# Performance work log

Measured on AMD Instinct MI355X. Metric: run time of the kernel, lower is better.

## Reference

```python
import jax, jax.numpy as jnp
import numpy as np

B, S, D, H = 64, 512, 1024, 1024


def setup_inputs() -> dict:
    key = jax.random.key(0)
    k1, k2, k3 = jax.random.split(key, 3)
    scale = 1.0 / np.sqrt(H)
    U = jax.random.normal(k1, (B, S, D), dtype=jnp.float32)
    W_ih = jax.random.normal(k2, (3 * H, D), dtype=jnp.float32) * scale
    W_hh = jax.random.normal(k3, (3 * H, H), dtype=jnp.float32) * scale
    b_ih = jnp.zeros((3 * H,), dtype=jnp.float32)
    b_hh = jnp.zeros((3 * H,), dtype=jnp.float32)
    return {"U": U, "W_ih": W_ih, "W_hh": W_hh, "b_ih": b_ih, "b_hh": b_hh}


def _gru_scan(U, W_ih, W_hh, b_ih, b_hh):
    # Precompute input-side gate projections for all timesteps: [B,S,3H]
    x_gates = jnp.einsum('bsd,gd->bsg', U, W_ih) + b_ih
    x_gates = jnp.transpose(x_gates, (1, 0, 2))  # [S,B,3H] for scan
    h0 = jnp.zeros((U.shape[0], W_hh.shape[1]), dtype=U.dtype)

    def step(h, xg):
        hg = h @ W_hh.T + b_hh  # [B,3H]
        xr, xz, xn = jnp.split(xg, 3, axis=-1)
        hr, hz, hn = jnp.split(hg, 3, axis=-1)
        r = jax.nn.sigmoid(xr + hr)
        z = jax.nn.sigmoid(xz + hz)
        n = jnp.tanh(xn + r * hn)
        h_new = (1.0 - z) * n + z * h
        return h_new, None

    h_final, _ = jax.lax.scan(step, h0, x_gates)
    return h_final  # [B,H]


def reference(U, W_ih, W_hh, b_ih, b_hh):
    # Dropout p=0.0 (eval-equivalent) -> identity, omitted.
    return _gru_scan(U, W_ih, W_hh, b_ih, b_hh)
```

## Files before the change

kernel.cpp:

```cpp
#include <hip/hip_runtime.h>

#define S_LEN 512
#define BATCH 64
#define HDIM  1024
#define GDIM  3072

typedef __attribute__((ext_vector_type(8))) short bf16x8;
typedef __attribute__((ext_vector_type(4))) float f32x4;
typedef __attribute__((ext_vector_type(4))) unsigned short u16x4;

__device__ inline unsigned short f2bf(float f) {
  unsigned u = __builtin_bit_cast(unsigned, f);
  u += 0x7fffu + ((u >> 16) & 1u);
  return (unsigned short)(u >> 16);
}
__device__ inline float bf2f(unsigned short h) {
  unsigned u = ((unsigned)h) << 16;
  return __builtin_bit_cast(float, u);
}
__device__ inline bf16x8 pack8(float4 a, float4 b) {
  bf16x8 r;
  r[0] = (short)f2bf(a.x); r[1] = (short)f2bf(a.y);
  r[2] = (short)f2bf(a.z); r[3] = (short)f2bf(a.w);
  r[4] = (short)f2bf(b.x); r[5] = (short)f2bf(b.y);
  r[6] = (short)f2bf(b.z); r[7] = (short)f2bf(b.w);
  return r;
}

__global__ __launch_bounds__(256, 2) void xg_gemm(
    const float* __restrict__ U, const float* __restrict__ Wih,
    const float* __restrict__ bih, unsigned short* __restrict__ xg) {
  __shared__ bf16x8 Asub[512];
  __shared__ bf16x8 Bsub[512];

  const int bid = blockIdx.x;
  const int nt = bid % 24;
  const int mt = bid / 24;
  const int tid = threadIdx.x;
  const int wave = tid >> 6, lane = tid & 63;
  const int q = lane >> 4, l15 = lane & 15;
  const int wm = wave >> 1, wn = wave & 1;

  const int srow = tid >> 1, shalf = tid & 1;
  const int arow = mt * 128 + srow;
  const float* Ag = U + ((size_t)(arow & 63) * S_LEN + (arow >> 6)) * HDIM + shalf * 16;
  const float* Bg = Wih + (size_t)(nt * 128 + srow) * HDIM + shalf * 16;
  const int sw = (srow >> 1) & 3;
  const int slot0 = srow * 4 + ((shalf * 2) ^ sw);
  const int slot1 = srow * 4 + ((shalf * 2 + 1) ^ sw);

  f32x4 acc[4][4];
#pragma unroll
  for (int i = 0; i < 4; ++i)
#pragma unroll
    for (int j = 0; j < 4; ++j) acc[i][j] = (f32x4){0.f, 0.f, 0.f, 0.f};

  for (int kk = 0; kk < 32; ++kk) {
    const float4* ap = (const float4*)(Ag + kk * 32);
    float4 a0 = ap[0], a1 = ap[1], a2 = ap[2], a3 = ap[3];
    const float4* bp = (const float4*)(Bg + kk * 32);
    float4 b0 = bp[0], b1 = bp[1], b2 = bp[2], b3 = bp[3];
    Asub[slot0] = pack8(a0, a1);
    Asub[slot1] = pack8(a2, a3);
    Bsub[slot0] = pack8(b0, b1);
    Bsub[slot1] = pack8(b2, b3);
    __syncthreads();
    bf16x8 af[4], bfr[4];
#pragma unroll
    for (int i = 0; i < 4; ++i) {
      int ar = wm * 64 + i * 16 + l15;
      af[i] = Asub[ar * 4 + (q ^ ((ar >> 1) & 3))];
      int br = wn * 64 + i * 16 + l15;
      bfr[i] = Bsub[br * 4 + (q ^ ((br >> 1) & 3))];
    }
#pragma unroll
    for (int i = 0; i < 4; ++i)
#pragma unroll
      for (int j = 0; j < 4; ++j)
        acc[i][j] = __builtin_amdgcn_mfma_f32_16x16x32_bf16(af[i], bfr[j], acc[i][j], 0, 0, 0);
    __syncthreads();
  }

#pragma unroll
  for (int j = 0; j < 4; ++j) {
    int gcol = nt * 128 + wn * 64 + j * 16 + l15;
    float bias = bih[gcol];
#pragma unroll
    for (int i = 0; i < 4; ++i) {
      int rbase = mt * 128 + wm * 64 + i * 16 + q * 4;
      int s = rbase >> 6;
      int b0i = rbase & 63;
      u16x4 pk;
#pragma unroll
      for (int r = 0; r < 4; ++r) pk[r] = f2bf(acc[i][j][r] + bias);
      *(u16x4*)(xg + ((size_t)s * GDIM + gcol) * BATCH + b0i) = pk;
    }
  }
}

__global__ __launch_bounds__(256, 1) void gru_scan(
    const float* __restrict__ Whh, const float* __restrict__ bhh,
    const unsigned short* __restrict__ xg, unsigned short* __restrict__ hbuf,
    unsigned int* __restrict__ flags, float* __restrict__ out) {
  __shared__ unsigned short h_stage[4][64 * 256];
  __shared__ float hown[64][16];
  __shared__ float bh_lds[3][16];

  const int p = blockIdx.x;
  const int j0 = p * 16;
  const int tid = threadIdx.x;
  const int w = tid >> 6, lane = tid & 63;
  const int q = lane >> 4, l15 = lane & 15;
  const int k0 = w * 256;
  const int cb = tid >> 2;
  const int cmq = (tid & 3) * 4;

  const int i2 = lane >> 5;
  const int cpos = lane & 31;

  bf16x8 wf[3][8];
#pragma unroll
  for (int g = 0; g < 3; ++g) {
    const float* wrow = Whh + ((size_t)g * HDIM + j0 + l15) * HDIM + k0;
#pragma unroll
    for (int kk = 0; kk < 8; ++kk) {
      const float4* wp = (const float4*)(wrow + kk * 32 + q * 8);
      wf[g][kk] = pack8(wp[0], wp[1]);
    }
  }
  if (tid < 48) bh_lds[tid >> 4][tid & 15] = bhh[(tid >> 4) * HDIM + j0 + (tid & 15)];
  { float4 z = {0.f, 0.f, 0.f, 0.f}; *(float4*)&hown[cb][cmq] = z; }
  __syncthreads();

  unsigned short xq[3][4];
#pragma unroll
  for (int g = 0; g < 3; ++g)
#pragma unroll
    for (int r = 0; r < 4; ++r)
      xq[g][r] = xg[((size_t)g * HDIM + j0 + cmq + r) * BATCH + cb];

  for (int t = 0; t < S_LEN; ++t) {
    const unsigned short* hcur = hbuf + (size_t)(t & 1) * (BATCH * HDIM);
    unsigned short* hnxt = hbuf + (size_t)((t + 1) & 1) * (BATCH * HDIM);

    {
      const unsigned short* hsrc = hcur + k0;
#pragma unroll
      for (int i = 0; i < 32; ++i) {
        const int b = 2 * i + i2;
        const int gch = cpos ^ (b & 7);
        const unsigned short* g = hsrc + (size_t)b * HDIM + gch * 8;
        __builtin_amdgcn_global_load_lds(
            (const __attribute__((address_space(1))) void*)g,
            (__attribute__((address_space(3))) void*)(&h_stage[w][i * 512]),
            16, 0, 0);
      }
    }
    asm volatile("s_waitcnt vmcnt(0)" ::: "memory");
    __builtin_amdgcn_sched_barrier(0);

    f32x4 acc[3][4];
#pragma unroll
    for (int g = 0; g < 3; ++g)
#pragma unroll
      for (int bt = 0; bt < 4; ++bt) acc[g][bt] = (f32x4){0.f, 0.f, 0.f, 0.f};

    const unsigned short* hl = h_stage[w];
#pragma unroll
    for (int kk = 0; kk < 8; ++kk) {
      const int csw = (((kk * 4 + q) ^ (l15 & 7)) * 8);
      bf16x8 h0 = *(const bf16x8*)(hl + (l15)      * 256 + csw);
      bf16x8 h1 = *(const bf16x8*)(hl + (16 + l15) * 256 + csw);
      bf16x8 h2 = *(const bf16x8*)(hl + (32 + l15) * 256 + csw);
      bf16x8 h3 = *(const bf16x8*)(hl + (48 + l15) * 256 + csw);
#pragma unroll
      for (int g = 0; g < 3; ++g) {
        acc[g][0] = __builtin_amdgcn_mfma_f32_16x16x32_bf16(wf[g][kk], h0, acc[g][0], 0, 0, 0);
        acc[g][1] = __builtin_amdgcn_mfma_f32_16x16x32_bf16(wf[g][kk], h1, acc[g][1], 0, 0, 0);
        acc[g][2] = __builtin_amdgcn_mfma_f32_16x16x32_bf16(wf[g][kk], h2, acc[g][2], 0, 0, 0);
        acc[g][3] = __builtin_amdgcn_mfma_f32_16x16x32_bf16(wf[g][kk], h3, acc[g][3], 0, 0, 0);
      }
    }
    __builtin_amdgcn_sched_barrier(0);

    {
      float* pw = (float*)(void*)h_stage[w];
      asm volatile("" : "+v"(pw));
#pragma unroll
      for (int g = 0; g < 3; ++g)
#pragma unroll
        for (int bt = 0; bt < 4; ++bt)
#pragma unroll
          for (int r = 0; r < 4; ++r)
            pw[(g * 16 + q * 4 + r) * 66 + bt * 16 + l15] = acc[g][bt][r];
    }
    __syncthreads();

    {
      float4 hv = *(float4*)&hown[cb][cmq];
      u16x4 pk;
#pragma unroll
      for (int r = 0; r < 4; ++r) {
        int m = cmq + r;
        float hr = bh_lds[0][m], hz = bh_lds[1][m], hn = bh_lds[2][m];
#pragma unroll
        for (int ww = 0; ww < 4; ++ww) {
          const float* pp = (const float*)(const void*)h_stage[ww];
          hr += pp[( 0 + m) * 66 + cb];
          hz += pp[(16 + m) * 66 + cb];
          hn += pp[(32 + m) * 66 + cb];
        }
        float xr = bf2f(xq[0][r]), xz = bf2f(xq[1][r]), xn = bf2f(xq[2][r]);
        float rr = 1.f / (1.f + __expf(-(xr + hr)));
        float zz = 1.f / (1.f + __expf(-(xz + hz)));
        float ex = __expf(2.f * (xn + rr * hn));
        float nn = 1.f - 2.f / (ex + 1.f);
        float hold = (r == 0) ? hv.x : (r == 1) ? hv.y : (r == 2) ? hv.z : hv.w;
        float hnew = (1.f - zz) * nn + zz * hold;
        if (r == 0) hv.x = hnew; else if (r == 1) hv.y = hnew; else if (r == 2) hv.z = hnew; else hv.w = hnew;
        pk[r] = f2bf(hnew);
      }
      *(float4*)&hown[cb][cmq] = hv;
      if (t + 1 < S_LEN) {
        __hip_atomic_store((unsigned long long*)(hnxt + (size_t)cb * HDIM + j0 + cmq),
                           __builtin_bit_cast(unsigned long long, pk),
                           __ATOMIC_RELAXED, __HIP_MEMORY_SCOPE_AGENT);
      }
    }
    __syncthreads();

    if (t + 1 < S_LEN) {
      if (tid == 0)
        __hip_atomic_store(&flags[p], (unsigned)(t + 1),
                           __ATOMIC_RELAXED, __HIP_MEMORY_SCOPE_AGENT);
#pragma unroll
      for (int g = 0; g < 3; ++g)
#pragma unroll
        for (int r = 0; r < 4; ++r)
          xq[g][r] = xg[((size_t)(t + 1) * GDIM + g * HDIM + j0 + cmq + r) * BATCH + cb];
      if (tid < 64) {
        unsigned spins = 0;
        while (__hip_atomic_load(&flags[tid], __ATOMIC_RELAXED, __HIP_MEMORY_SCOPE_AGENT)
               < (unsigned)(t + 1)) {
          __builtin_amdgcn_s_sleep(1);
          if (++spins > 50000000u) break;
        }
      }
      __syncthreads();
      __builtin_amdgcn_fence(__ATOMIC_ACQUIRE, "agent");
    }
  }

  *(float4*)(out + (size_t)cb * HDIM + j0 + cmq) = *(float4*)&hown[cb][cmq];
}

extern "C" void kernel_launch(void* const* d_in, const int* in_sizes, int n_in,
                              void* d_out, int out_size, void* d_ws, size_t ws_size,
                              hipStream_t stream) {
  const float* U   = (const float*)d_in[0];
  const float* Wih = (const float*)d_in[1];
  const float* Whh = (const float*)d_in[2];
  const float* bih = (const float*)d_in[3];
  const float* bhh = (const float*)d_in[4];
  float* out = (float*)d_out;

  char* ws = (char*)d_ws;
  const size_t XG_BYTES = (size_t)S_LEN * GDIM * BATCH * 2;
  unsigned short* xg   = (unsigned short*)ws;
  unsigned short* hbuf = (unsigned short*)(ws + XG_BYTES);
  const size_t H_BYTES = (size_t)2 * BATCH * HDIM * 2;
  unsigned int* flags  = (unsigned int*)(ws + XG_BYTES + H_BYTES);

  hipMemsetAsync(ws + XG_BYTES, 0, H_BYTES + 256, stream);

  hipLaunchKernelGGL(xg_gemm, dim3((32768 / 128) * (GDIM / 128)), dim3(256), 0, stream,
                     U, Wih, bih, xg);
  hipLaunchKernelGGL(gru_scan, dim3(64), dim3(256), 0, stream,
                     Whh, bhh, xg, hbuf, flags, out);
}
```

Measured before the change: 4.113 ms.

## Split GRU recurrence K-dimension across eight waves with coherent register-staged h loads

The recurrent scan kernel now runs 512 threads, so each of eight waves handles a 128-wide slice of the hidden K dimension instead of 256. The goal is to halve each wave's serial MFMA chain and load volume on the critical path of every timestep. The previous h staging used global_load_lds; it is replaced with inline-asm global_load_dwordx4 carrying sc0 sc1 cache-coherence bits, followed by swizzled LDS stores. Because those loads bypass stale caches, the agent acquire fence is dropped. The per-thread hidden state now lives in registers instead of LDS. The cost is a wider cross-wave reduction over eight partial sums in the gate epilogue, and threads 256 to 511 sit idle during that epilogue.

Result: faster. 3.483 ms (-15.3%).

```diff
diff --git a/kernel.cpp b/kernel.cpp
--- a/kernel.cpp
+++ b/kernel.cpp
@@ -98,12 +98,11 @@
   }
 }
 
-__global__ __launch_bounds__(256, 1) void gru_scan(
+__global__ __launch_bounds__(512, 1) void gru_scan(
     const float* __restrict__ Whh, const float* __restrict__ bhh,
     const unsigned short* __restrict__ xg, unsigned short* __restrict__ hbuf,
     unsigned int* __restrict__ flags, float* __restrict__ out) {
-  __shared__ unsigned short h_stage[4][64 * 256];
-  __shared__ float hown[64][16];
+  __shared__ unsigned short hls[8 * 8192];
   __shared__ float bh_lds[3][16];
 
   const int p = blockIdx.x;
@@ -111,26 +110,27 @@
   const int tid = threadIdx.x;
   const int w = tid >> 6, lane = tid & 63;
   const int q = lane >> 4, l15 = lane & 15;
-  const int k0 = w * 256;
+  const int k0 = w * 128;
   const int cb = tid >> 2;
   const int cmq = (tid & 3) * 4;
 
-  const int i2 = lane >> 5;
-  const int cpos = lane & 31;
-
-  bf16x8 wf[3][8];
+  const int srow0 = lane >> 4;
+  const int sc = lane & 15;
+
+  bf16x8 wf[3][4];
 #pragma unroll
   for (int g = 0; g < 3; ++g) {
     const float* wrow = Whh + ((size_t)g * HDIM + j0 + l15) * HDIM + k0;
 #pragma unroll
-    for (int kk = 0; kk < 8; ++kk) {
+    for (int kk = 0; kk < 4; ++kk) {
       const float4* wp = (const float4*)(wrow + kk * 32 + q * 8);
       wf[g][kk] = pack8(wp[0], wp[1]);
     }
   }
   if (tid < 48) bh_lds[tid >> 4][tid & 15] = bhh[(tid >> 4) * HDIM + j0 + (tid & 15)];
-  { float4 z = {0.f, 0.f, 0.f, 0.f}; *(float4*)&hown[cb][cmq] = z; }
   __syncthreads();
+
+  float4 hv = {0.f, 0.f, 0.f, 0.f};
 
   unsigned short xq[3][4];
 #pragma unroll
@@ -139,52 +139,96 @@
     for (int r = 0; r < 4; ++r)
       xq[g][r] = xg[((size_t)g * HDIM + j0 + cmq + r) * BATCH + cb];
 
+  const size_t HS = (size_t)BATCH * HDIM;
+
   for (int t = 0; t < S_LEN; ++t) {
-    const unsigned short* hcur = hbuf + (size_t)(t & 1) * (BATCH * HDIM);
-    unsigned short* hnxt = hbuf + (size_t)((t + 1) & 1) * (BATCH * HDIM);
+    const unsigned short* hcur = hbuf + (size_t)(t & 1) * HS;
+    unsigned short* hnxt = hbuf + (size_t)((t + 1) & 1) * HS;
 
     {
-      const unsigned short* hsrc = hcur + k0;
-#pragma unroll
-      for (int i = 0; i < 32; ++i) {
-        const int b = 2 * i + i2;
-        const int gch = cpos ^ (b & 7);
-        const unsigned short* g = hsrc + (size_t)b * HDIM + gch * 8;
-        __builtin_amdgcn_global_load_lds(
-            (const __attribute__((address_space(1))) void*)g,
-            (__attribute__((address_space(3))) void*)(&h_stage[w][i * 512]),
-            16, 0, 0);
-      }
-    }
-    asm volatile("s_waitcnt vmcnt(0)" ::: "memory");
+      const unsigned short* gb = hcur + (size_t)srow0 * HDIM + k0 + sc * 8;
+      const unsigned short *g0 = gb,            *g1 = gb + 4 * HDIM,
+                           *g2 = gb + 8 * HDIM, *g3 = gb + 12 * HDIM,
+                           *g4 = gb + 16 * HDIM,*g5 = gb + 20 * HDIM,
+                           *g6 = gb + 24 * HDIM,*g7 = gb + 28 * HDIM;
+      bf16x8 v0, v1, v2, v3, v4, v5, v6, v7;
+      asm volatile(
+          "global_load_dwordx4 %0, %8, off sc0 sc1\n\t"
+          "global_load_dwordx4 %1, %9, off sc0 sc1\n\t"
+          "global_load_dwordx4 %2, %10, off sc0 sc1\n\t"
+          "global_load_dwordx4 %3, %11, off sc0 sc1\n\t"
+          "global_load_dwordx4 %4, %12, off sc0 sc1\n\t"
+          "global_load_dwordx4 %5, %13, off sc0 sc1\n\t"
+          "global_load_dwordx4 %6, %14, off sc0 sc1\n\t"
+          "global_load_dwordx4 %7, %15, off sc0 sc1"
+          : "=&v"(v0), "=&v"(v1), "=&v"(v2), "=&v"(v3),
+            "=&v"(v4), "=&v"(v5), "=&v"(v6), "=&v"(v7)
+          : "v"(g0), "v"(g1), "v"(g2), "v"(g3),
+            "v"(g4), "v"(g5), "v"(g6), "v"(g7));
+      const unsigned short *g8 = gb + 32 * HDIM, *g9 = gb + 36 * HDIM,
+                           *gA = gb + 40 * HDIM, *gB = gb + 44 * HDIM,
+                           *gC = gb + 48 * HDIM, *gD = gb + 52 * HDIM,
+                           *gE = gb + 56 * HDIM, *gF = gb + 60 * HDIM;
+      bf16x8 v8, v9, vA, vB, vC, vD, vE, vF;
+      asm volatile(
+          "global_load_dwordx4 %0, %8, off sc0 sc1\n\t"
+          "global_load_dwordx4 %1, %9, off sc0 sc1\n\t"
+          "global_load_dwordx4 %2, %10, off sc0 sc1\n\t"
+          "global_load_dwordx4 %3, %11, off sc0 sc1\n\t"
+          "global_load_dwordx4 %4, %12, off sc0 sc1\n\t"
+          "global_load_dwordx4 %5, %13, off sc0 sc1\n\t"
+          "global_load_dwordx4 %6, %14, off sc0 sc1\n\t"
+          "global_load_dwordx4 %7, %15, off sc0 sc1"
+          : "=&v"(v8), "=&v"(v9), "=&v"(vA), "=&v"(vB),
+            "=&v"(vC), "=&v"(vD), "=&v"(vE), "=&v"(vF)
+          : "v"(g8), "v"(g9), "v"(gA), "v"(gB),
+            "v"(gC), "v"(gD), "v"(gE), "v"(gF));
+
+#define STW(J, VV)                                                        \
+      {                                                                   \
+        const int row_ = srow0 + 4 * (J);                                 \
+        const int c2_ = (sc & 8) | ((sc ^ row_) & 7);                     \
+        *(bf16x8*)&hls[w * 8192 + row_ * 128 + c2_ * 8] = (VV);           \
+      }
+      asm volatile("s_waitcnt vmcnt(8)" ::: "memory");
+      __builtin_amdgcn_sched_barrier(0);
+      STW(0, v0) STW(1, v1) STW(2, v2) STW(3, v3)
+      STW(4, v4) STW(5, v5) STW(6, v6) STW(7, v7)
+      asm volatile("s_waitcnt vmcnt(0)" ::: "memory");
+      __builtin_amdgcn_sched_barrier(0);
+      STW(8, v8) STW(9, v9) STW(10, vA) STW(11, vB)
+      STW(12, vC) STW(13, vD) STW(14, vE) STW(15, vF)
+#undef STW
+    }
+
+    f32x4 acc[3][4];
+#pragma unroll
+    for (int g = 0; g < 3; ++g)
+#pragma unroll
+      for (int bt = 0; bt < 4; ++bt) acc[g][bt] = (f32x4){0.f, 0.f, 0.f, 0.f};
+
+#pragma unroll
+    for (int kk = 0; kk < 4; ++kk) {
+      const int c = kk * 4 + q;
+      bf16x8 hB[4];
+#pragma unroll
+      for (int bt = 0; bt < 4; ++bt) {
+        const int row = bt * 16 + l15;
+        const int c2 = (c & 8) | ((c ^ row) & 7);
+        hB[bt] = *(const bf16x8*)&hls[w * 8192 + row * 128 + c2 * 8];
+      }
+#pragma unroll
+      for (int g = 0; g < 3; ++g) {
+        acc[g][0] = __builtin_amdgcn_mfma_f32_16x16x32_bf16(wf[g][kk], hB[0], acc[g][0], 0, 0, 0);
+        acc[g][1] = __builtin_amdgcn_mfma_f32_16x16x32_bf16(wf[g][kk], hB[1], acc[g][1], 0, 0, 0);
+        acc[g][2] = __builtin_amdgcn_mfma_f32_16x16x32_bf16(wf[g][kk], hB[2], acc[g][2], 0, 0, 0);
+        acc[g][3] = __builtin_amdgcn_mfma_f32_16x16x32_bf16(wf[g][kk], hB[3], acc[g][3], 0, 0, 0);
+      }
+    }
     __builtin_amdgcn_sched_barrier(0);
 
-    f32x4 acc[3][4];
-#pragma unroll
-    for (int g = 0; g < 3; ++g)
-#pragma unroll
-      for (int bt = 0; bt < 4; ++bt) acc[g][bt] = (f32x4){0.f, 0.f, 0.f, 0.f};
-
-    const unsigned short* hl = h_stage[w];
-#pragma unroll
-    for (int kk = 0; kk < 8; ++kk) {
-      const int csw = (((kk * 4 + q) ^ (l15 & 7)) * 8);
-      bf16x8 h0 = *(const bf16x8*)(hl + (l15)      * 256 + csw);
-      bf16x8 h1 = *(const bf16x8*)(hl + (16 + l15) * 256 + csw);
-      bf16x8 h2 = *(const bf16x8*)(hl + (32 + l15) * 256 + csw);
-      bf16x8 h3 = *(const bf16x8*)(hl + (48 + l15) * 256 + csw);
-#pragma unroll
-      for (int g = 0; g < 3; ++g) {
-        acc[g][0] = __builtin_amdgcn_mfma_f32_16x16x32_bf16(wf[g][kk], h0, acc[g][0], 0, 0, 0);
-        acc[g][1] = __builtin_amdgcn_mfma_f32_16x16x32_bf16(wf[g][kk], h1, acc[g][1], 0, 0, 0);
-        acc[g][2] = __builtin_amdgcn_mfma_f32_16x16x32_bf16(wf[g][kk], h2, acc[g][2], 0, 0, 0);
-        acc[g][3] = __builtin_amdgcn_mfma_f32_16x16x32_bf16(wf[g][kk], h3, acc[g][3], 0, 0, 0);
-      }
-    }
-    __builtin_amdgcn_sched_barrier(0);
-
     {
-      float* pw = (float*)(void*)h_stage[w];
+      float* pw = (float*)&hls[w * 8192];
       asm volatile("" : "+v"(pw));
 #pragma unroll
       for (int g = 0; g < 3; ++g)
@@ -196,16 +240,15 @@
     }
     __syncthreads();
 
-    {
-      float4 hv = *(float4*)&hown[cb][cmq];
+    if (tid < 256) {
       u16x4 pk;
 #pragma unroll
       for (int r = 0; r < 4; ++r) {
         int m = cmq + r;
         float hr = bh_lds[0][m], hz = bh_lds[1][m], hn = bh_lds[2][m];
 #pragma unroll
-        for (int ww = 0; ww < 4; ++ww) {
-          const float* pp = (const float*)(const void*)h_stage[ww];
+        for (int ww = 0; ww < 8; ++ww) {
+          const float* pp = (const float*)&hls[ww * 8192];
           hr += pp[( 0 + m) * 66 + cb];
           hz += pp[(16 + m) * 66 + cb];
           hn += pp[(32 + m) * 66 + cb];
@@ -220,7 +263,6 @@
         if (r == 0) hv.x = hnew; else if (r == 1) hv.y = hnew; else if (r == 2) hv.z = hnew; else hv.w = hnew;
         pk[r] = f2bf(hnew);
       }
-      *(float4*)&hown[cb][cmq] = hv;
       if (t + 1 < S_LEN) {
         __hip_atomic_store((unsigned long long*)(hnxt + (size_t)cb * HDIM + j0 + cmq),
                            __builtin_bit_cast(unsigned long long, pk),
@@ -247,11 +289,11 @@
         }
       }
       __syncthreads();
-      __builtin_amdgcn_fence(__ATOMIC_ACQUIRE, "agent");
     }
   }
 
-  *(float4*)(out + (size_t)cb * HDIM + j0 + cmq) = *(float4*)&hown[cb][cmq];
+  if (tid < 256)
+    *(float4*)(out + (size_t)cb * HDIM + j0 + cmq) = hv;
 }
 
 extern "C" void kernel_launch(void* const* d_in, const int* in_sizes, int n_in,
@@ -275,6 +317,6 @@
 
   hipLaunchKernelGGL(xg_gemm, dim3((32768 / 128) * (GDIM / 128)), dim3(256), 0, stream,
                      U, Wih, bih, xg);
-  hipLaunchKernelGGL(gru_scan, dim3(64), dim3(256), 0, stream,
+  hipLaunchKernelGGL(gru_scan, dim3(64), dim3(512), 0, stream,
                      Whh, bhh, xg, hbuf, flags, out);
 }
```
